# Performance work log

Hardware: AMD Instinct MI355X
Metric: run time of the kernel (lower is better)

The kernel has to match this reference:

```python
import jax, jax.numpy as jnp
import numpy as np

B, H, W = 128, 48, 48
CEN_IN, CEN_OUT, DIR_IN, DIR_OUT, CEN_K, DIR_K = 32, 32, 24, 24, 3, 5
C_IN = CEN_IN + 4 * DIR_IN  # central + 4 directional groups (hor, ver, diag, anti-diag)


def _dwconv(x, k):
    # x: [B, C, H, W], k: [C, kh, kw] depthwise kernels -> SAME-padded depthwise conv
    C = x.shape[1]
    return jax.lax.conv_general_dilated(
        x, k[:, None], window_strides=(1, 1), padding='SAME',
        dimension_numbers=('NCHW', 'OIHW', 'NCHW'), feature_group_count=C)


def setup_inputs() -> dict:
    key = jax.random.key(0)
    ks = jax.random.split(key, 8)
    s = 0.1
    return {
        'x': jax.random.normal(ks[0], (B, C_IN, H, W), dtype=jnp.float32),
        'cen_tensor': jax.random.normal(ks[1], (CEN_IN, CEN_K, CEN_K), dtype=jnp.float32) * s,
        'dir_tensor': jax.random.normal(ks[2], (DIR_IN, DIR_K), dtype=jnp.float32) * s,
        'cen2cen': jax.random.normal(ks[3], (CEN_OUT, CEN_IN), dtype=jnp.float32) * s,
        'par2cen': jax.random.normal(ks[4], (CEN_OUT, DIR_IN), dtype=jnp.float32) * s,
        'dia2cen': jax.random.normal(ks[5], (CEN_OUT, DIR_IN), dtype=jnp.float32) * s,
        'cen2dir': jax.random.normal(ks[6], (DIR_OUT, CEN_IN), dtype=jnp.float32) * s,
        'dir2dir': jax.random.normal(ks[7], (DIR_OUT, DIR_IN), dtype=jnp.float32) * s,
    }


def reference(x, cen_tensor, dir_tensor, cen2cen, par2cen, dia2cen, cen2dir, dir2dir):
    cen_in = cen_tensor.shape[0]
    dir_in, K = dir_tensor.shape
    # split channel groups: [cen | hor | ver | diag | anti-diag]
    xc = x[:, :cen_in]
    xh = x[:, cen_in:cen_in + dir_in]
    xv = x[:, cen_in + dir_in:cen_in + 2 * dir_in]
    xd1 = x[:, cen_in + 2 * dir_in:cen_in + 3 * dir_in]
    xd2 = x[:, cen_in + 3 * dir_in:]
    eye = jnp.eye(K, dtype=x.dtype)
    # --- directional depthwise stage ---
    yc = _dwconv(xc, cen_tensor)                                # full 2D kernel per channel
    yh = _dwconv(xh, dir_tensor[:, None, :])
    yv = _dwconv(xv, dir_tensor[:, :, None])                    # K x 1 vertical line
    yd1 = _dwconv(xd1, dir_tensor[:, :, None] * eye)            # main diagonal line
    yd2 = _dwconv(xd2, dir_tensor[:, :, None] * eye[:, ::-1])   # anti-diagonal line
    # --- directional pointwise (1x1) mixing stage ---
    mix = lambda Wm, t: jnp.einsum('oc,bchw->bohw', Wm, t)
    out_cen = mix(cen2cen, yc) + mix(par2cen, yh + yv) + mix(dia2cen, yd1 + yd2)
    od_cen = mix(cen2dir, yc)
    out_dirs = [od_cen + mix(dir2dir, t) for t in (yh, yv, yd1, yd2)]
    return jnp.concatenate([out_cen] + out_dirs, axis=1)
```

## Files before the change

kernel.cpp:

```cpp
#include <hip/hip_runtime.h>
#include <hip/hip_bf16.h>


namespace {
constexpr int HH = 48, WW = 48, HW = HH * WW;
constexpr int C_IN = 128, C_OUT = 128, NB = 128;
constexpr int RPB = 8;
constexpr int NSTR = HH / RPB;
constexpr int PIX = RPB * WW;
constexpr int NT = 512;
constexpr int CHK = 16;
constexpr int NCHK = C_IN / CHK;
constexpr int XR = RPB + 4;
constexpr int XW = 64;
constexpr size_t M_BYTES = 128 * 128 * 2;
constexpr size_t ZB_OFF = M_BYTES;
}

typedef __attribute__((ext_vector_type(8))) short bf16x8;
typedef __attribute__((ext_vector_type(4))) float f32x4;

__device__ __forceinline__ ushort f2bf(float f) {
    __hip_bfloat16 h = __float2bfloat16(f);
    return *reinterpret_cast<ushort*>(&h);
}

__global__ void build_M(const float* __restrict__ c2c, const float* __restrict__ p2c,
                        const float* __restrict__ d2c, const float* __restrict__ c2d,
                        const float* __restrict__ d2dW, ushort* __restrict__ Mbf) {
    int t = blockIdx.x * 256 + threadIdx.x;
    if (t >= 128 * 128) return;
    int o = t & 127, c = t >> 7;
    float v;
    if (o < 32) {
        if (c < 32)       v = c2c[o * 32 + c];
        else if (c < 56)  v = p2c[o * 24 + c - 32];
        else if (c < 80)  v = p2c[o * 24 + c - 56];
        else if (c < 104) v = d2c[o * 24 + c - 80];
        else              v = d2c[o * 24 + c - 104];
    } else {
        int g = (o - 32) / 24, oo = (o - 32) % 24;
        if (c < 32) v = c2d[oo * 32 + c];
        else {
            int gc = (c - 32) / 24, cc2 = (c - 32) % 24;
            v = (gc == g) ? d2dW[oo * 24 + cc2] : 0.f;
        }
    }
    Mbf[o * 128 + c] = f2bf(v);
}

__global__ __launch_bounds__(NT) void dsc_fused(
    const float* __restrict__ x,
    const float* __restrict__ cen_t,
    const float* __restrict__ dir_t,
    const ushort* __restrict__ Mbf,
    const float* __restrict__ zb,
    float* __restrict__ out)
{
    __shared__ float  xs[CHK][XR][XW];
    __shared__ ushort yT[PIX * 128];
    __shared__ ushort ycp[CHK][PIX];

    const int tid = threadIdx.x;
    const int b   = blockIdx.x / NSTR;
    const int h0  = (blockIdx.x % NSTR) * RPB;
    const float* __restrict__ xb = x + (size_t)b * C_IN * HW;

    auto stage = [&](int t) {
        const int c0 = t * CHK;
#pragma unroll
        for (int k = 0; k < 6; ++k) {
            int i  = tid + k * NT;
            int q  = i & 15;
            int rc = i >> 4;
            int r  = rc % XR;
            int c  = rc / XR;
            int gh = h0 - 2 + r;
            bool ok = ((unsigned)gh < (unsigned)HH) && (q < 12);
            const float* src = ok ? (xb + (size_t)(c0 + c) * HW + gh * WW + q * 4) : zb;
            __builtin_amdgcn_global_load_lds(
                (const __attribute__((address_space(1))) unsigned int*)src,
                (__attribute__((address_space(3))) unsigned int*)(&xs[0][0][0] + (size_t)i * 4),
                16, 0, 0);
        }
    };

    auto dwconv = [&](int t) {
        const int c0 = t * CHK;
#pragma unroll
        for (int k = 0; k < 3; ++k) {
            int task = tid + k * NT;
            int c    = task / 96;
            int rem  = task % 96;
            int row  = rem / 12;
            int w0   = (rem % 12) * 4;
            int cc   = c0 + c;
            float o0 = 0.f, o1 = 0.f, o2 = 0.f, o3 = 0.f;
            if (cc < 32) {
#pragma unroll
                for (int i = 0; i < 3; ++i) {
                    float v[6];
#pragma unroll
                    for (int j = 0; j < 6; ++j) v[j] = xs[c][row + 1 + i][(w0 + j - 1) & 63];
                    float k0 = cen_t[cc * 9 + i * 3 + 0];
                    float k1 = cen_t[cc * 9 + i * 3 + 1];
                    float k2 = cen_t[cc * 9 + i * 3 + 2];
                    o0 += k0 * v[0] + k1 * v[1] + k2 * v[2];
                    o1 += k0 * v[1] + k1 * v[2] + k2 * v[3];
                    o2 += k0 * v[2] + k1 * v[3] + k2 * v[4];
                    o3 += k0 * v[3] + k1 * v[4] + k2 * v[5];
                }
            } else if (cc < 56) {
                int cd = cc - 32;
                float v[8];
#pragma unroll
                for (int j = 0; j < 8; ++j) v[j] = xs[c][row + 2][(w0 + j - 2) & 63];
#pragma unroll
                for (int i = 0; i < 5; ++i) {
                    float tt = dir_t[cd * 5 + i];
                    o0 += tt * v[i]; o1 += tt * v[i + 1]; o2 += tt * v[i + 2]; o3 += tt * v[i + 3];
                }
            } else if (cc < 80) {
                int cd = cc - 56;
#pragma unroll
                for (int i = 0; i < 5; ++i) {
                    float tt = dir_t[cd * 5 + i];
                    float4 vq = *(const float4*)&xs[c][row + i][w0];
                    o0 += tt * vq.x; o1 += tt * vq.y; o2 += tt * vq.z; o3 += tt * vq.w;
                }
            } else if (cc < 104) {
                int cd = cc - 80;
#pragma unroll
                for (int i = 0; i < 5; ++i) {
                    float tt = dir_t[cd * 5 + i];
                    int base = w0 + i - 2;
                    o0 += tt * xs[c][row + i][(base + 0) & 63];
                    o1 += tt * xs[c][row + i][(base + 1) & 63];
                    o2 += tt * xs[c][row + i][(base + 2) & 63];
                    o3 += tt * xs[c][row + i][(base + 3) & 63];
                }
            } else {
                int cd = cc - 104;
#pragma unroll
                for (int i = 0; i < 5; ++i) {
                    float tt = dir_t[cd * 5 + i];
                    int base = w0 + 2 - i;
                    o0 += tt * xs[c][row + i][(base + 0) & 63];
                    o1 += tt * xs[c][row + i][(base + 1) & 63];
                    o2 += tt * xs[c][row + i][(base + 2) & 63];
                    o3 += tt * xs[c][row + i][(base + 3) & 63];
                }
            }
            int p = row * 48 + w0;
            ushort4 s = {f2bf(o0), f2bf(o1), f2bf(o2), f2bf(o3)};
            *(ushort4*)&ycp[c][p] = s;
        }
    };

    auto transpose = [&](int t) {
        const int c0 = t * CHK;
#pragma unroll
        for (int k = 0; k < 3; ++k) {
            int t2 = tid + k * NT;
            int cq = t2 / PIX;
            int p  = t2 % PIX;
            ushort4 s;
            s.x = ycp[cq * 4 + 0][p];
            s.y = ycp[cq * 4 + 1][p];
            s.z = ycp[cq * 4 + 2][p];
            s.w = ycp[cq * 4 + 3][p];
            int byte = (p << 8) + ((c0 + cq * 4) << 1);
            byte ^= (p & 7) << 4;
            *(ushort4*)((char*)yT + byte) = s;
        }
    };

    stage(0);
    __syncthreads();
    for (int t = 0; t < NCHK; ++t) {
        dwconv(t);
        __syncthreads();
        if (t + 1 < NCHK) stage(t + 1);
        transpose(t);
        __syncthreads();
    }

    const int l     = tid & 63;
    const int wv    = tid >> 6;
    const int ofr   = wv & 3;
    const int phalf = wv >> 2;
    float* __restrict__ ob = out + (size_t)b * C_OUT * HW + h0 * WW;

#pragma unroll
    for (int pass = 0; pass < 2; ++pass) {
        int o0 = pass * 64 + ofr * 16;
        bf16x8 afr[4];
#pragma unroll
        for (int kb = 0; kb < 4; ++kb)
            afr[kb] = *(const bf16x8*)(Mbf + (o0 + (l & 15)) * 128 + kb * 32 + (l >> 4) * 8);
        f32x4 acc[12] = {};
#pragma unroll
        for (int kb = 0; kb < 4; ++kb)
#pragma unroll
            for (int pf = 0; pf < 12; ++pf) {
                int p = (phalf * 12 + pf) * 16 + (l & 15);
                int byte = (p << 8) + ((kb * 32 + (l >> 4) * 8) << 1);
                byte ^= (p & 7) << 4;
                bf16x8 bfr = *(const bf16x8*)((const char*)yT + byte);
                acc[pf] = __builtin_amdgcn_mfma_f32_16x16x32_bf16(afr[kb], bfr, acc[pf], 0, 0, 0);
            }
#pragma unroll
        for (int pf = 0; pf < 12; ++pf) {
            int p = (phalf * 12 + pf) * 16 + (l & 15);
            int obase = o0 + (l >> 4) * 4;
#pragma unroll
            for (int r = 0; r < 4; ++r)
                ob[(size_t)(obase + r) * HW + p] = acc[pf][r];
        }
    }
}

extern "C" void kernel_launch(void* const* d_in, const int* in_sizes, int n_in,
                              void* d_out, int out_size, void* d_ws, size_t ws_size,
                              hipStream_t stream) {
    const float* x     = (const float*)d_in[0];
    const float* cen_t = (const float*)d_in[1];
    const float* dir_t = (const float*)d_in[2];
    const float* c2c   = (const float*)d_in[3];
    const float* p2c   = (const float*)d_in[4];
    const float* d2c   = (const float*)d_in[5];
    const float* c2d   = (const float*)d_in[6];
    const float* d2dW  = (const float*)d_in[7];
    float* out = (float*)d_out;

    ushort* Mbf = (ushort*)d_ws;
    float*  zb  = (float*)((char*)d_ws + ZB_OFF);

    hipMemsetAsync(zb, 0, 64, stream);
    build_M<<<64, 256, 0, stream>>>(c2c, p2c, d2c, c2d, d2dW, Mbf);
    dsc_fused<<<NB * NSTR, NT, 0, stream>>>(x, cen_t, dir_t, Mbf, zb, out);
}
```

Baseline: 103.2 us.

## Double-buffer input staging with smaller channel chunks and padded LDS layouts

Halves the channel chunk size and adds two shared-memory input buffers, so the global-to-LDS load of the next chunk is issued before the depthwise convolution of the current one and overlaps with it. The input tile is compacted to a 17-quad row stride instead of 64 floats, and the transposed activation buffer now uses padded strides (136 and 392 elements) in place of the XOR swizzle. The transpose becomes scalar per-element stores. This removes the serial load-then-compute step per chunk but doubles the number of chunk iterations and barriers, and the padded stride may change LDS bank conflicts in the MFMA B-fragment reads.

```diff
diff --git a/kernel.cpp b/kernel.cpp
--- a/kernel.cpp
+++ b/kernel.cpp
@@ -9,10 +9,13 @@
 constexpr int NSTR = HH / RPB;
 constexpr int PIX = RPB * WW;
 constexpr int NT = 512;
-constexpr int CHK = 16;
+constexpr int CHK = 8;
 constexpr int NCHK = C_IN / CHK;
 constexpr int XR = RPB + 4;
-constexpr int XW = 64;
+constexpr int QR = 17;
+constexpr int XQ = CHK * XR * QR;
+constexpr int YTS = 136;
+constexpr int YCS = 392;
 constexpr size_t M_BYTES = 128 * 128 * 2;
 constexpr size_t ZB_OFF = M_BYTES;
 }
@@ -57,51 +60,56 @@
     const float* __restrict__ zb,
     float* __restrict__ out)
 {
-    __shared__ float  xs[CHK][XR][XW];
-    __shared__ ushort yT[PIX * 128];
-    __shared__ ushort ycp[CHK][PIX];
+    __shared__ float  xs[2][XQ * 4];
+    __shared__ ushort yT[PIX * YTS];
+    __shared__ ushort ycp[CHK * YCS];
 
     const int tid = threadIdx.x;
     const int b   = blockIdx.x / NSTR;
     const int h0  = (blockIdx.x % NSTR) * RPB;
     const float* __restrict__ xb = x + (size_t)b * C_IN * HW;
 
-    auto stage = [&](int t) {
+    auto stage = [&](int t, int buf) {
         const int c0 = t * CHK;
 #pragma unroll
-        for (int k = 0; k < 6; ++k) {
-            int i  = tid + k * NT;
-            int q  = i & 15;
-            int rc = i >> 4;
-            int r  = rc % XR;
-            int c  = rc / XR;
-            int gh = h0 - 2 + r;
-            bool ok = ((unsigned)gh < (unsigned)HH) && (q < 12);
-            const float* src = ok ? (xb + (size_t)(c0 + c) * HW + gh * WW + q * 4) : zb;
-            __builtin_amdgcn_global_load_lds(
-                (const __attribute__((address_space(1))) unsigned int*)src,
-                (__attribute__((address_space(3))) unsigned int*)(&xs[0][0][0] + (size_t)i * 4),
-                16, 0, 0);
+        for (int k = 0; k < 4; ++k) {
+            int d = tid + k * NT;
+            if (d < XQ) {
+                int q  = d % QR;
+                int cr = d / QR;
+                int r  = cr % XR;
+                int c  = cr / XR;
+                int gh = h0 - 2 + r;
+                bool ok = ((unsigned)gh < (unsigned)HH) && (q < 12);
+                const float* src = ok ? (xb + (size_t)(c0 + c) * HW + gh * WW + q * 4) : zb;
+                __builtin_amdgcn_global_load_lds(
+                    (const __attribute__((address_space(1))) unsigned int*)src,
+                    (__attribute__((address_space(3))) unsigned int*)(&xs[buf][0] + (size_t)d * 4),
+                    16, 0, 0);
+            }
         }
     };
 
-    auto dwconv = [&](int t) {
+    auto dwconv = [&](int t, int buf) {
         const int c0 = t * CHK;
 #pragma unroll
-        for (int k = 0; k < 3; ++k) {
+        for (int k = 0; k < 2; ++k) {
             int task = tid + k * NT;
+            if (task >= CHK * 96) break;
             int c    = task / 96;
             int rem  = task % 96;
             int row  = rem / 12;
             int w0   = (rem % 12) * 4;
             int cc   = c0 + c;
             float o0 = 0.f, o1 = 0.f, o2 = 0.f, o3 = 0.f;
+#define XROW(i_) (&xs[buf][(size_t)((c * XR + row + (i_)) * QR) * 4])
             if (cc < 32) {
 #pragma unroll
                 for (int i = 0; i < 3; ++i) {
+                    const float* xr = XROW(i + 1);
                     float v[6];
 #pragma unroll
-                    for (int j = 0; j < 6; ++j) v[j] = xs[c][row + 1 + i][(w0 + j - 1) & 63];
+                    for (int j = 0; j < 6; ++j) v[j] = xr[(w0 + j - 1) & 63];
                     float k0 = cen_t[cc * 9 + i * 3 + 0];
                     float k1 = cen_t[cc * 9 + i * 3 + 1];
                     float k2 = cen_t[cc * 9 + i * 3 + 2];
@@ -112,9 +120,10 @@
                 }
             } else if (cc < 56) {
                 int cd = cc - 32;
+                const float* xr = XROW(2);
                 float v[8];
 #pragma unroll
-                for (int j = 0; j < 8; ++j) v[j] = xs[c][row + 2][(w0 + j - 2) & 63];
+                for (int j = 0; j < 8; ++j) v[j] = xr[(w0 + j - 2) & 63];
 #pragma unroll
                 for (int i = 0; i < 5; ++i) {
                     float tt = dir_t[cd * 5 + i];
@@ -125,7 +134,7 @@
 #pragma unroll
                 for (int i = 0; i < 5; ++i) {
                     float tt = dir_t[cd * 5 + i];
-                    float4 vq = *(const float4*)&xs[c][row + i][w0];
+                    float4 vq = *(const float4*)&XROW(i)[w0];
                     o0 += tt * vq.x; o1 += tt * vq.y; o2 += tt * vq.z; o3 += tt * vq.w;
                 }
             } else if (cc < 104) {
@@ -133,54 +142,50 @@
 #pragma unroll
                 for (int i = 0; i < 5; ++i) {
                     float tt = dir_t[cd * 5 + i];
+                    const float* xr = XROW(i);
                     int base = w0 + i - 2;
-                    o0 += tt * xs[c][row + i][(base + 0) & 63];
-                    o1 += tt * xs[c][row + i][(base + 1) & 63];
-                    o2 += tt * xs[c][row + i][(base + 2) & 63];
-                    o3 += tt * xs[c][row + i][(base + 3) & 63];
+                    o0 += tt * xr[(base + 0) & 63];
+                    o1 += tt * xr[(base + 1) & 63];
+                    o2 += tt * xr[(base + 2) & 63];
+                    o3 += tt * xr[(base + 3) & 63];
                 }
             } else {
                 int cd = cc - 104;
 #pragma unroll
                 for (int i = 0; i < 5; ++i) {
                     float tt = dir_t[cd * 5 + i];
+                    const float* xr = XROW(i);
                     int base = w0 + 2 - i;
-                    o0 += tt * xs[c][row + i][(base + 0) & 63];
-                    o1 += tt * xs[c][row + i][(base + 1) & 63];
-                    o2 += tt * xs[c][row + i][(base + 2) & 63];
-                    o3 += tt * xs[c][row + i][(base + 3) & 63];
+                    o0 += tt * xr[(base + 0) & 63];
+                    o1 += tt * xr[(base + 1) & 63];
+                    o2 += tt * xr[(base + 2) & 63];
+                    o3 += tt * xr[(base + 3) & 63];
                 }
             }
+#undef XROW
             int p = row * 48 + w0;
             ushort4 s = {f2bf(o0), f2bf(o1), f2bf(o2), f2bf(o3)};
-            *(ushort4*)&ycp[c][p] = s;
+            *(ushort4*)&ycp[c * YCS + p] = s;
         }
     };
 
     auto transpose = [&](int t) {
         const int c0 = t * CHK;
-#pragma unroll
-        for (int k = 0; k < 3; ++k) {
-            int t2 = tid + k * NT;
-            int cq = t2 / PIX;
-            int p  = t2 % PIX;
-            ushort4 s;
-            s.x = ycp[cq * 4 + 0][p];
-            s.y = ycp[cq * 4 + 1][p];
-            s.z = ycp[cq * 4 + 2][p];
-            s.w = ycp[cq * 4 + 3][p];
-            int byte = (p << 8) + ((c0 + cq * 4) << 1);
-            byte ^= (p & 7) << 4;
-            *(ushort4*)((char*)yT + byte) = s;
+        const int c  = tid & 7;
+        const int pp = tid >> 3;
+#pragma unroll
+        for (int j = 0; j < 6; ++j) {
+            int p = pp + 64 * j;
+            yT[p * YTS + c0 + c] = ycp[c * YCS + p];
         }
     };
 
-    stage(0);
+    stage(0, 0);
     __syncthreads();
     for (int t = 0; t < NCHK; ++t) {
-        dwconv(t);
+        if (t + 1 < NCHK) stage(t + 1, (t + 1) & 1);
+        dwconv(t, t & 1);
         __syncthreads();
-        if (t + 1 < NCHK) stage(t + 1);
         transpose(t);
         __syncthreads();
     }
@@ -204,9 +209,7 @@
 #pragma unroll
             for (int pf = 0; pf < 12; ++pf) {
                 int p = (phalf * 12 + pf) * 16 + (l & 15);
-                int byte = (p << 8) + ((kb * 32 + (l >> 4) * 8) << 1);
-                byte ^= (p & 7) << 4;
-                bf16x8 bfr = *(const bf16x8*)((const char*)yT + byte);
+                bf16x8 bfr = *(const bf16x8*)&yT[p * YTS + kb * 32 + (l >> 4) * 8];
                 acc[pf] = __builtin_amdgcn_mfma_f32_16x16x32_bf16(afr[kb], bfr, acc[pf], 0, 0, 0);
             }
 #pragma unroll
```

Result: slower. 125.9 us (+22.0%).
